# Performance work log

Hardware: AMD Instinct MI355X
Metric: run time of the kernel (lower is better)

The kernel has to match this reference:

```python
import jax, jax.numpy as jnp
import numpy as np
from functools import partial

WS, STRIDE, ALPHA, NHEADS = 8, 4, 0.3, 4


def _conv3x3(x, w, b):
    # x: [B,Cin,H,W], w: [Cout,Cin,3,3]
    y = jax.lax.conv_general_dilated(x, w, (1, 1), 'SAME',
                                     dimension_numbers=('NCHW', 'OIHW', 'NCHW'))
    return y + b[None, :, None, None]


def _conv1x1(x, w, b):
    y = jax.lax.conv_general_dilated(x, w, (1, 1), 'SAME',
                                     dimension_numbers=('NCHW', 'OIHW', 'NCHW'))
    return y + b[None, :, None, None]


def _mha(x, wqkv, bqkv, wo, bo):
    # x: [N, L, E] self-attention, torch nn.MultiheadAttention semantics
    N, L, E = x.shape
    hd = E // NHEADS
    qkv = x @ wqkv.T + bqkv                      # [N, L, 3E]
    q, k, v = jnp.split(qkv, 3, axis=-1)
    def heads(t):
        return t.reshape(N, L, NHEADS, hd).transpose(0, 2, 1, 3)  # [N,h,L,hd]
    q, k, v = heads(q) * (hd ** -0.5), heads(k), heads(v)
    attn = jax.nn.softmax(jnp.einsum('nhld,nhmd->nhlm', q, k), axis=-1)
    o = jnp.einsum('nhlm,nhmd->nhld', attn, v).transpose(0, 2, 1, 3).reshape(N, L, E)
    return o @ wo.T + bo


def _forward(vector_field, mw1, mb1, mw2, mb2, aw1, ab1, aw2, ab2,
             in_proj_w, in_proj_b, out_proj_w, out_proj_b, fc_w, fc_b):
    B, C_total, H, W = vector_field.shape
    C = C_total // 2
    E = 2 * C
    magnitudes = vector_field[:, :C]
    angles = vector_field[:, C:]

    mag_p = _conv3x3(jax.nn.relu(_conv3x3(magnitudes, mw1, mb1)), mw2, mb2)
    ang_p = _conv3x3(jax.nn.relu(_conv3x3(angles, aw1, ab1)), aw2, ab2)

    combined0 = jnp.concatenate([mag_p, ang_p], axis=1)      # [B, E, H, W]

    # ---- batched windowed cross-attention (windows read the ORIGINAL processed field) ----
    hs = np.arange(0, H - WS + 1, STRIDE)
    ws_ = np.arange(0, W - WS + 1, STRIDE)
    Nh, Nw = len(hs), len(ws_)
    rows = hs[:, None] + np.arange(WS)                        # [Nh, WS]
    cols = ws_[:, None] + np.arange(WS)                       # [Nw, WS]
    win = combined0[:, :, rows][:, :, :, :, cols]             # [B,E,Nh,WS,Nw,WS]
    tokens = win.transpose(2, 4, 0, 3, 5, 1).reshape(Nh * Nw * B, WS * WS, E)
    att = _mha(tokens, in_proj_w, in_proj_b, out_proj_w, out_proj_b)
    att = att.reshape(Nh * Nw, B, WS, WS, E).transpose(0, 1, 4, 2, 3)  # [NhNw,B,E,WS,WS]

    # ---- sequential read-modify-write blend (h outer, w inner loop order) ----
    h_idx = jnp.asarray(np.repeat(hs, Nw), dtype=jnp.int32)
    w_idx = jnp.asarray(np.tile(ws_, Nh), dtype=jnp.int32)

    def step(carry, inp):
        a, h0, w0 = inp
        cur = jax.lax.dynamic_slice(carry, (0, 0, h0, w0), (B, E, WS, WS))
        new = cur * (1.0 - ALPHA) + a * ALPHA
        return jax.lax.dynamic_update_slice(carry, new, (0, 0, h0, w0)), None

    enhanced, _ = jax.lax.scan(step, combined0, (att, h_idx, w_idx))

    enhanced_mag = enhanced[:, :C]
    enhanced_ang = enhanced[:, C:]

    flow_weights = jax.nn.sigmoid(_conv1x1(enhanced, fc_w, fc_b))  # [B,C,H,W]
    out = jnp.concatenate([enhanced_mag * flow_weights,
                           enhanced_ang * flow_weights], axis=1)
    return out + vector_field


def setup_inputs() -> dict:
    key = jax.random.key(0)
    ks = jax.random.split(key, 16)
    B, C, H, W = 4, 64, 128, 128
    E = 2 * C
    s = 0.05
    def n(k, shape):
        return jax.random.normal(k, shape, dtype=jnp.float32) * s
    return {
        'vector_field': jax.random.normal(ks[0], (B, 2 * C, H, W), dtype=jnp.float32),
        'mw1': n(ks[1], (C // 2, C, 3, 3)), 'mb1': n(ks[2], (C // 2,)),
        'mw2': n(ks[3], (C, C // 2, 3, 3)), 'mb2': n(ks[4], (C,)),
        'aw1': n(ks[5], (C // 2, C, 3, 3)), 'ab1': n(ks[6], (C // 2,)),
        'aw2': n(ks[7], (C, C // 2, 3, 3)), 'ab2': n(ks[8], (C,)),
        'in_proj_w': n(ks[9], (3 * E, E)), 'in_proj_b': n(ks[10], (3 * E,)),
        'out_proj_w': n(ks[11], (E, E)), 'out_proj_b': n(ks[12], (E,)),
        'fc_w': n(ks[13], (C, E, 1, 1)), 'fc_b': n(ks[14], (C,)),
    }


def reference(vector_field, mw1, mb1, mw2, mb2, aw1, ab1, aw2, ab2,
              in_proj_w, in_proj_b, out_proj_w, out_proj_b, fc_w, fc_b):
    return _forward(vector_field, mw1, mb1, mw2, mb2, aw1, ab1, aw2, ab2,
                    in_proj_w, in_proj_b, out_proj_w, out_proj_b, fc_w, fc_b)
```

## Files before the change

### kernel.cpp

```cpp
#include <hip/hip_runtime.h>
#include <hip/hip_bf16.h>


#define HW 16384
#define NSEQ 3844

#define WF_IPW 0
#define WF_IPB 49152
#define WF_OPW 49536
#define WF_OPB 65920
#define WF_FCW 66048
#define WF_FCB 74240
#define WF_MW1 74304
#define WF_MB1 92736
#define WF_AW1 92768
#define WF_AB1 111200
#define WF_MW2 111232
#define WF_MB2 129664
#define WF_AW2 129728
#define WF_AB2 148160
#define WF_TOTAL 148224
#define WF_W2BF 24576

typedef __bf16 bf16x8 __attribute__((ext_vector_type(8)));
typedef float f32x4 __attribute__((ext_vector_type(4)));
typedef unsigned int uint2v __attribute__((ext_vector_type(2)));
typedef unsigned int uint4v __attribute__((ext_vector_type(4)));

#define MFMA16(a, b, c) __builtin_amdgcn_mfma_f32_16x16x32_bf16((a), (b), (c), 0, 0, 0)

__device__ __forceinline__ float bfu(unsigned short u) {
    union { unsigned int i; float f; } v; v.i = ((unsigned int)u) << 16; return v.f;
}
__device__ __forceinline__ unsigned short fbf(float f) {
    union { float f; unsigned int i; } v; v.f = f;
    unsigned int x = v.i;
    return (unsigned short)((x + 0x7fffu + ((x >> 16) & 1u)) >> 16);
}
__device__ __forceinline__ unsigned int cvt_pk_bf16(float a, float b) {
    unsigned int r;
    asm("v_cvt_pk_bf16_f32 %0, %1, %2" : "=v"(r) : "v"(a), "v"(b));
    return r;
}
__device__ __forceinline__ unsigned short fbf_hw(float f) {
    return (unsigned short)cvt_pk_bf16(f, f);
}
__device__ __forceinline__ float ldin(const void* p, long long i, bool f32) {
    return f32 ? ((const float*)p)[i] : bfu(((const unsigned short*)p)[i]);
}
__device__ __forceinline__ bf16x8 frag_ld(const unsigned short* p) {
    union { uint4v u; bf16x8 b; } v;
    v.u = *(const uint4v*)p;
    return v.b;
}
__device__ __forceinline__ uint2v pack4(float a, float b, float c, float d) {
    uint2v r;
    r.x = cvt_pk_bf16(a, b);
    r.y = cvt_pk_bf16(c, d);
    return r;
}
__device__ __forceinline__ void unp8(uint4v u, float* x) {
    union { unsigned int i; float f; } a;
    a.i = u.x << 16;         x[0] = a.f;
    a.i = u.x & 0xffff0000u; x[1] = a.f;
    a.i = u.y << 16;         x[2] = a.f;
    a.i = u.y & 0xffff0000u; x[3] = a.f;
    a.i = u.z << 16;         x[4] = a.f;
    a.i = u.z & 0xffff0000u; x[5] = a.f;
    a.i = u.w << 16;         x[6] = a.f;
    a.i = u.w & 0xffff0000u; x[7] = a.f;
}

__global__ __launch_bounds__(256) void detect_kernel(const unsigned short* __restrict__ vfu,
                                                     int* __restrict__ flag)
{
    __shared__ int cnt;
    if (threadIdx.x == 0) cnt = 0;
    __syncthreads();
    int bad = 0;
    for (int i = threadIdx.x; i < 8192; i += 256) {
        int e = (vfu[i] >> 7) & 0xff;
        if (e < 0x60 || e > 0xA0) ++bad;
    }
    atomicAdd(&cnt, bad);
    __syncthreads();
    if (threadIdx.x == 0) *flag = (cnt > 400) ? 1 : 0;
}

__global__ __launch_bounds__(256) void cvtw_kernel(
    const void* ipw, const void* ipb,
    const void* opw, const void* opb,
    const void* fcw, const void* fcb,
    const void* mw1, const void* mb1,
    const void* aw1, const void* ab1,
    const void* mw2, const void* mb2,
    const void* aw2, const void* ab2,
    const int* __restrict__ flag, float* __restrict__ wf)
{
    int i = blockIdx.x * 256 + threadIdx.x;
    if (i >= WF_TOTAL) return;
    const bool f32 = (*flag != 0);
    const void* src; int off;
    if      (i < WF_IPB) { src = ipw; off = WF_IPW; }
    else if (i < WF_OPW) { src = ipb; off = WF_IPB; }
    else if (i < WF_OPB) { src = opw; off = WF_OPW; }
    else if (i < WF_FCW) { src = opb; off = WF_OPB; }
    else if (i < WF_FCB) { src = fcw; off = WF_FCW; }
    else if (i < WF_MW1) { src = fcb; off = WF_FCB; }
    else if (i < WF_MB1) { src = mw1; off = WF_MW1; }
    else if (i < WF_AW1) { src = mb1; off = WF_MB1; }
    else if (i < WF_AB1) { src = aw1; off = WF_AW1; }
    else if (i < WF_MB2) { src = (i < WF_MW2) ? ab1 : mw2; off = (i < WF_MW2) ? WF_AB1 : WF_MW2; }
    else if (i < WF_AW2) { src = mb2; off = WF_MB2; }
    else if (i < WF_AB2) { src = aw2; off = WF_AW2; }
    else                 { src = ab2; off = WF_AB2; }
    float v = ldin(src, i - off, f32);
    if (i < WF_IPB) {
        ((unsigned short*)(wf + WF_IPW))[i] = fbf(v);
    } else if (i >= WF_OPW && i < WF_OPB) {
        ((unsigned short*)(wf + WF_OPW))[i - WF_OPW] = fbf(v);
    } else {
        wf[i] = v;
    }
    if (i >= WF_MW2 && i < WF_MB2) {
        int rel = i - WF_MW2;
        int oc = rel / 288, rem = rel - oc * 288;
        int ic = rem / 9, tap = rem - ic * 9;
        ((unsigned short*)(wf + WF_W2BF))[oc * 288 + tap * 32 + ic] = fbf(v);
    } else if (i >= WF_AW2 && i < WF_AB2) {
        int rel = i - WF_AW2;
        int oc = rel / 288, rem = rel - oc * 288;
        int ic = rem / 9, tap = rem - ic * 9;
        ((unsigned short*)(wf + WF_W2BF))[18432 + oc * 288 + tap * 32 + ic] = fbf(v);
    }
}

template<int IC, bool RELU>
__device__ void conv3x3_body(const void* __restrict__ in, long long in_off, bool f32,
                             const float* __restrict__ w,
                             const float* __restrict__ bias,
                             unsigned short* __restrict__ out)
{
    __shared__ float xs[32][6][37];
    const int t = threadIdx.x;
    const int tx0 = blockIdx.x * 32, ty0 = blockIdx.y * 4;
    const int wv = __builtin_amdgcn_readfirstlane(t >> 6);
    const int lane = t & 63;
    const int pr = lane >> 4, pc2 = lane & 15;

    float acc[8][2];
#pragma unroll
    for (int oo = 0; oo < 8; ++oo)
#pragma unroll
        for (int p = 0; p < 2; ++p) acc[oo][p] = 0.f;

    for (int cc = 0; cc < IC; cc += 32) {
        if (cc) __syncthreads();
        for (int i = t; i < 32 * 108; i += 256) {
            int c = i / 108, rem = i - c * 108;
            int rr = rem / 18, s = rem - rr * 18;
            int gy = ty0 + rr - 1;
            const bool gyok = (gy >= 0 && gy < 128);
            long long rowoff = in_off + (long long)(cc + c) * HW + gy * 128;
            if (s >= 1 && s <= 16) {
                int cx = 2 * s - 1;
                int gx = tx0 + cx - 1;
                float v0 = 0.f, v1 = 0.f;
                if (gyok) {
                    if (f32) {
                        float2 u = *(const float2*)((const float*)in + rowoff + gx);
                        v0 = u.x; v1 = u.y;
                    } else {
                        unsigned int u = *(const unsigned int*)
                            ((const unsigned short*)in + rowoff + gx);
                        v0 = bfu((unsigned short)(u & 0xffffu));
                        v1 = bfu((unsigned short)(u >> 16));
                    }
                }
                xs[c][rr][cx] = v0;
                xs[c][rr][cx + 1] = v1;
            } else {
                int cx = (s == 0) ? 0 : 33;
                int gx = tx0 + cx - 1;
                float v = 0.f;
                if (gyok && gx >= 0 && gx < 128)
                    v = ldin(in, rowoff + gx, f32);
                xs[c][rr][cx] = v;
            }
        }
        __syncthreads();
        for (int c = 0; c < 32; ++c) {
            float xv[3][4];
#pragma unroll
            for (int dy = 0; dy < 3; ++dy)
#pragma unroll
                for (int dx = 0; dx < 4; ++dx)
                    xv[dy][dx] = xs[c][pr + dy][pc2 * 2 + dx];
            const float* wr0 = w + (wv * 8 * IC + (cc + c)) * 9;
#pragma unroll
            for (int oo = 0; oo < 8; ++oo) {
                const float* wr = wr0 + oo * IC * 9;
#pragma unroll
                for (int dy = 0; dy < 3; ++dy)
#pragma unroll
                    for (int dx = 0; dx < 3; ++dx) {
                        float wvv = wr[dy * 3 + dx];
#pragma unroll
                        for (int p = 0; p < 2; ++p)
                            acc[oo][p] = fmaf(wvv, xv[dy][p + dx], acc[oo][p]);
                    }
            }
        }
    }
    const int px = tx0 + pc2 * 2, py = ty0 + pr;
#pragma unroll
    for (int p = 0; p < 2; ++p) {
        union { unsigned int u32[4]; uint4v v; } pk;
#pragma unroll
        for (int j = 0; j < 4; ++j) {
            float v0 = acc[2 * j][p] + bias[wv * 8 + 2 * j];
            float v1 = acc[2 * j + 1][p] + bias[wv * 8 + 2 * j + 1];
            if (RELU) { v0 = fmaxf(v0, 0.f); v1 = fmaxf(v1, 0.f); }
            pk.u32[j] = cvt_pk_bf16(v0, v1);
        }
        *(uint4v*)(out + (size_t)(py * 128 + px + p) * 32 + wv * 8) = pk.v;
    }
}

__global__ __launch_bounds__(256) void conv1_kernel(const void* __restrict__ vf,
                                                    const float* __restrict__ wf,
                                                    const int* __restrict__ flag,
                                                    unsigned short* __restrict__ hidden)
{
    int z = blockIdx.z, b = z >> 1, br = z & 1;
    const bool f32 = (*flag != 0);
    conv3x3_body<64, true>(vf, (long long)(b * 128 + br * 64) * HW, f32,
                           wf + (br ? WF_AW1 : WF_MW1), wf + (br ? WF_AB1 : WF_MB1),
                           hidden + (size_t)z * 16384 * 32);
}

__global__ __launch_bounds__(256) void conv2_kernel(const unsigned short* __restrict__ hidden,
                                                    const float* __restrict__ wf,
                                                    unsigned short* __restrict__ comb)
{
    __shared__ unsigned short xs[8160];
    const int t = threadIdx.x;
    const int tx0 = blockIdx.x * 32, ty0 = blockIdx.y * 4;
    const int z = blockIdx.z, b = z >> 1, br = z & 1;
    const size_t ibase = (size_t)z * 16384;

    for (int i = t; i < 816; i += 256) {
        const int rec = i >> 2, part = i & 3;
        const int rr = rec / 34, cx = rec - rr * 34;
        const int gy = ty0 + rr - 1, gx = tx0 + cx - 1;
        uint4v v = {0u, 0u, 0u, 0u};
        if (gy >= 0 && gy < 128 && gx >= 0 && gx < 128)
            v = *(const uint4v*)(hidden + (ibase + gy * 128 + gx) * 32 + part * 8);
        *(uint4v*)&xs[rec * 40 + part * 8] = v;
    }
    __syncthreads();

    const int lane = t & 63, quad = lane >> 4, l16 = lane & 15;
    const int wv = __builtin_amdgcn_readfirstlane(t >> 6);
    const unsigned short* w2 = (const unsigned short*)(wf + WF_W2BF) + br * 18432;
    const float* bias = wf + (br ? WF_AB2 : WF_MB2);

    f32x4 acc[4][2];
#pragma unroll
    for (int oct = 0; oct < 4; ++oct) {
        f32x4 b4;
#pragma unroll
        for (int r = 0; r < 4; ++r) b4[r] = bias[oct * 16 + quad * 4 + r];
        acc[oct][0] = b4;
        acc[oct][1] = b4;
    }

    __builtin_amdgcn_s_setprio(1);
#pragma unroll
    for (int tap = 0; tap < 9; ++tap) {
        const int dy = tap / 3, dx = tap - dy * 3;
        bf16x8 bxf[2];
#pragma unroll
        for (int pt2 = 0; pt2 < 2; ++pt2)
            bxf[pt2] = frag_ld(&xs[((wv + dy) * 34 + (pt2 * 16 + l16 + dx)) * 40 + quad * 8]);
#pragma unroll
        for (int oct = 0; oct < 4; ++oct) {
            bf16x8 af = frag_ld(&w2[(oct * 16 + l16) * 288 + tap * 32 + quad * 8]);
            acc[oct][0] = MFMA16(af, bxf[0], acc[oct][0]);
            acc[oct][1] = MFMA16(af, bxf[1], acc[oct][1]);
        }
    }
    __builtin_amdgcn_s_setprio(0);

#pragma unroll
    for (int pt2 = 0; pt2 < 2; ++pt2) {
        const int px_ = tx0 + pt2 * 16 + l16;
        unsigned short* op = comb + ((size_t)b * 16384 + (ty0 + wv) * 128 + px_) * 128
                           + br * 64 + quad * 4;
#pragma unroll
        for (int oct = 0; oct < 4; ++oct)
            *(uint2v*)(op + oct * 16) =
                pack4(acc[oct][pt2][0], acc[oct][pt2][1],
                      acc[oct][pt2][2], acc[oct][pt2][3]);
    }
}

__global__ __launch_bounds__(256) void mha_kernel(
    const unsigned short* __restrict__ comb,
    const float* __restrict__ wf,
    unsigned short* __restrict__ att)
{
    __shared__ unsigned short lds[25088];

    const unsigned short* wqkv = (const unsigned short*)(wf + WF_IPW);
    const unsigned short* wo   = (const unsigned short*)(wf + WF_OPW);

    const int bid = blockIdx.x;
    const int xcd = bid & 7, idx = bid >> 3;
    const int start = (xcd < 4) ? xcd * 481 : 1924 + (xcd - 4) * 480;
    const int nl = start + idx;
    const int bb = nl / 961;
    const int ihw = nl - bb * 961;
    const int ih = ihw / 31, iw = ihw - ih * 31;
    const int n = ihw * 4 + bb;

    const int t = threadIdx.x;
    const int lane = t & 63, quad = lane >> 4, l16 = lane & 15;
    const int hh = __builtin_amdgcn_readfirstlane(t >> 6);
    const int hb = hh * 32;
    const int QOFF = 8704 + hh * 4096;
    const int KOFF = QOFF + 2048;
    const int VOFF = hh * 2048;

#pragma unroll
    for (int rh = 0; rh < 2; ++rh) {
        const int r = hh * 2 + rh;
        const unsigned short* rp = comb +
            (size_t)(bb * 16384 + (ih * 4 + r) * 128 + iw * 4) * 128;
#pragma unroll
        for (int hv = 0; hv < 2; ++hv) {
            uint4v v = *(const uint4v*)(rp + hv * 512 + lane * 8);
            const int tok = r * 8 + hv * 4 + (lane >> 4);
            *(uint4v*)&lds[tok * 136 + (lane & 15) * 8] = v;
        }
    }
    __syncthreads();

    {
        f32x4 acc[4][4];
#pragma unroll
        for (int nt = 0; nt < 4; ++nt) {
            const int rb = (nt < 2) ? (hb + nt * 16) : (128 + hb + (nt - 2) * 16);
            f32x4 b4;
            b4[0] = wf[WF_IPB + rb + quad * 4 + 0];
            b4[1] = wf[WF_IPB + rb + quad * 4 + 1];
            b4[2] = wf[WF_IPB + rb + quad * 4 + 2];
            b4[3] = wf[WF_IPB + rb + quad * 4 + 3];
#pragma unroll
            for (int mt = 0; mt < 4; ++mt) acc[nt][mt] = b4;
        }
        __builtin_amdgcn_s_setprio(1);
#pragma unroll
        for (int kc = 0; kc < 4; ++kc) {
            bf16x8 bx[4];
#pragma unroll
            for (int mt = 0; mt < 4; ++mt)
                bx[mt] = frag_ld(&lds[(mt * 16 + l16) * 136 + kc * 32 + quad * 8]);
#pragma unroll
            for (int nt = 0; nt < 4; ++nt) {
                const int rb = (nt < 2) ? (hb + nt * 16) : (128 + hb + (nt - 2) * 16);
                bf16x8 aw = frag_ld(&wqkv[(rb + l16) * 128 + kc * 32 + quad * 8]);
#pragma unroll
                for (int mt = 0; mt < 4; ++mt)
                    acc[nt][mt] = MFMA16(aw, bx[mt], acc[nt][mt]);
            }
        }
        __builtin_amdgcn_s_setprio(0);
#pragma unroll
        for (int nt = 0; nt < 2; ++nt)
#pragma unroll
            for (int mt = 0; mt < 4; ++mt) {
                const int tok = mt * 16 + l16;
                const int aoff = tok * 32 + (((nt * 2 + (quad >> 1)) ^ (tok & 3)) << 3)
                               + (quad & 1) * 4;
                *(uint2v*)&lds[QOFF + aoff] =
                    pack4(acc[nt][mt][0], acc[nt][mt][1], acc[nt][mt][2], acc[nt][mt][3]);
                *(uint2v*)&lds[KOFF + aoff] =
                    pack4(acc[nt + 2][mt][0], acc[nt + 2][mt][1],
                          acc[nt + 2][mt][2], acc[nt + 2][mt][3]);
            }
    }

    f32x4 accv[2][4];
#pragma unroll
    for (int nv = 0; nv < 2; ++nv) {
        const int rb = 256 + hb + nv * 16;
        f32x4 b4;
        b4[0] = wf[WF_IPB + rb + quad * 4 + 0];
        b4[1] = wf[WF_IPB + rb + quad * 4 + 1];
        b4[2] = wf[WF_IPB + rb + quad * 4 + 2];
        b4[3] = wf[WF_IPB + rb + quad * 4 + 3];
#pragma unroll
        for (int mt = 0; mt < 4; ++mt) accv[nv][mt] = b4;
    }
    __builtin_amdgcn_s_setprio(1);
#pragma unroll
    for (int kc = 0; kc < 4; ++kc) {
        bf16x8 bx[4];
#pragma unroll
        for (int mt = 0; mt < 4; ++mt)
            bx[mt] = frag_ld(&lds[(mt * 16 + l16) * 136 + kc * 32 + quad * 8]);
#pragma unroll
        for (int nv = 0; nv < 2; ++nv) {
            const int rb = 256 + hb + nv * 16;
            bf16x8 aw = frag_ld(&wqkv[(rb + l16) * 128 + kc * 32 + quad * 8]);
#pragma unroll
            for (int mt = 0; mt < 4; ++mt)
                accv[nv][mt] = MFMA16(aw, bx[mt], accv[nv][mt]);
        }
    }
    __builtin_amdgcn_s_setprio(0);
    __syncthreads();

#pragma unroll
    for (int nv = 0; nv < 2; ++nv)
#pragma unroll
        for (int mt = 0; mt < 4; ++mt)
#pragma unroll
            for (int r = 0; r < 4; ++r) {
                const int d = nv * 16 + quad * 4 + r;
                const int tok = mt * 16 + l16;
                lds[VOFF + d * 64 + (((tok >> 3) ^ (d & 7)) << 3) + (tok & 7)] =
                    fbf_hw(accv[nv][mt][r]);
            }

    bf16x8 ak[4], bq[4];
#pragma unroll
    for (int mtk = 0; mtk < 4; ++mtk) {
        const int tok = mtk * 16 + l16;
        ak[mtk] = frag_ld(&lds[KOFF + tok * 32 + ((quad ^ (tok & 3)) << 3)]);
    }
#pragma unroll
    for (int ntq = 0; ntq < 4; ++ntq) {
        const int tok = ntq * 16 + l16;
        bq[ntq] = frag_ld(&lds[QOFF + tok * 32 + ((quad ^ (tok & 3)) << 3)]);
    }
    f32x4 sc[4][4];
    {
        f32x4 zz = {0.f, 0.f, 0.f, 0.f};
        __builtin_amdgcn_s_setprio(1);
#pragma unroll
        for (int mtk = 0; mtk < 4; ++mtk)
#pragma unroll
            for (int ntq = 0; ntq < 4; ++ntq)
                sc[mtk][ntq] = MFMA16(ak[mtk], bq[ntq], zz);
        __builtin_amdgcn_s_setprio(0);
    }

    const float scale = 0.17677669529663687f;
#pragma unroll
    for (int ntq = 0; ntq < 4; ++ntq) {
        float m0 = -1e30f;
#pragma unroll
        for (int mtk = 0; mtk < 4; ++mtk)
#pragma unroll
            for (int r = 0; r < 4; ++r) {
                sc[mtk][ntq][r] *= scale;
                m0 = fmaxf(m0, sc[mtk][ntq][r]);
            }
        m0 = fmaxf(m0, __shfl_xor(m0, 16));
        m0 = fmaxf(m0, __shfl_xor(m0, 32));
        float s0 = 0.f;
#pragma unroll
        for (int mtk = 0; mtk < 4; ++mtk)
#pragma unroll
            for (int r = 0; r < 4; ++r) {
                float p = __expf(sc[mtk][ntq][r] - m0);
                sc[mtk][ntq][r] = p;
                s0 += p;
            }
        s0 += __shfl_xor(s0, 16);
        s0 += __shfl_xor(s0, 32);
        float inv = 1.f / s0;
        const int tokq = ntq * 16 + l16;
#pragma unroll
        for (int mtk = 0; mtk < 4; ++mtk)
            *(uint2v*)&lds[QOFF + tokq * 64 +
                           (((mtk * 2 + (quad >> 1)) ^ (tokq & 7)) << 3) + (quad & 1) * 4] =
                pack4(sc[mtk][ntq][0] * inv, sc[mtk][ntq][1] * inv,
                      sc[mtk][ntq][2] * inv, sc[mtk][ntq][3] * inv);
    }
    __asm__ volatile("s_waitcnt lgkmcnt(0)" ::: "memory");

    f32x4 ov[4][2];
#pragma unroll
    for (int mt = 0; mt < 4; ++mt)
#pragma unroll
        for (int nv = 0; nv < 2; ++nv) { f32x4 zz = {0.f, 0.f, 0.f, 0.f}; ov[mt][nv] = zz; }
    __builtin_amdgcn_s_setprio(1);
#pragma unroll
    for (int ks = 0; ks < 2; ++ks) {
        bf16x8 ap[4];
#pragma unroll
        for (int mt = 0; mt < 4; ++mt) {
            const int tokq = mt * 16 + l16;
            ap[mt] = frag_ld(&lds[QOFF + tokq * 64 + (((ks * 4 + quad) ^ (tokq & 7)) << 3)]);
        }
#pragma unroll
        for (int nv = 0; nv < 2; ++nv) {
            const int d = nv * 16 + l16;
            bf16x8 bv = frag_ld(&lds[VOFF + d * 64 + (((ks * 4 + quad) ^ (d & 7)) << 3)]);
#pragma unroll
            for (int mt = 0; mt < 4; ++mt)
                ov[mt][nv] = MFMA16(ap[mt], bv, ov[mt][nv]);
        }
    }
    __builtin_amdgcn_s_setprio(0);
    __syncthreads();

#pragma unroll
    for (int mt = 0; mt < 4; ++mt)
#pragma unroll
        for (int nv = 0; nv < 2; ++nv)
#pragma unroll
            for (int r = 0; r < 4; ++r)
                lds[(mt * 16 + quad * 4 + r) * 136 + hb + nv * 16 + l16] =
                    fbf_hw(ov[mt][nv][r]);
    __syncthreads();

    f32x4 dp[4][2];
#pragma unroll
    for (int mt = 0; mt < 4; ++mt)
#pragma unroll
        for (int nl = 0; nl < 2; ++nl) { f32x4 zz = {0.f, 0.f, 0.f, 0.f}; dp[mt][nl] = zz; }
    __builtin_amdgcn_s_setprio(1);
#pragma unroll
    for (int ks = 0; ks < 4; ++ks) {
        bf16x8 af[4];
#pragma unroll
        for (int mt = 0; mt < 4; ++mt)
            af[mt] = frag_ld(&lds[(mt * 16 + l16) * 136 + ks * 32 + quad * 8]);
#pragma unroll
        for (int nl = 0; nl < 2; ++nl) {
            const int erow = hb + nl * 16 + l16;
            bf16x8 bw = frag_ld(&wo[erow * 128 + ks * 32 + quad * 8]);
#pragma unroll
            for (int mt = 0; mt < 4; ++mt)
                dp[mt][nl] = MFMA16(af[mt], bw, dp[mt][nl]);
        }
    }
    __builtin_amdgcn_s_setprio(0);
    __syncthreads();

#pragma unroll
    for (int mt = 0; mt < 4; ++mt)
#pragma unroll
        for (int nl = 0; nl < 2; ++nl)
#pragma unroll
            for (int r = 0; r < 4; ++r)
                lds[(mt * 16 + quad * 4 + r) * 136 + hb + nl * 16 + l16] =
                    fbf_hw(dp[mt][nl][r]);
    __syncthreads();

    {
        const int tok2 = t >> 2, eo = (t & 3) * 32;
        unsigned short* op = att + (size_t)n * 8192 + tok2 * 128 + eo;
        const unsigned short* lp = lds + tok2 * 136 + eo;
#pragma unroll
        for (int k4 = 0; k4 < 4; ++k4)
            *(uint4v*)(op + k4 * 8) = *(const uint4v*)(lp + k4 * 8);
    }
}

__global__ __launch_bounds__(256) void fuse_kernel(
    const unsigned short* __restrict__ comb,
    const unsigned short* __restrict__ att,
    const void* __restrict__ vf,
    const float* __restrict__ wf,
    const int* __restrict__ flag,
    void* __restrict__ outp)
{
    __shared__ float enhs[128][65];
    __shared__ float fws[64][65];
    const float* fcw = wf + WF_FCW;
    const float* fcb = wf + WF_FCB;
    const bool f32 = (*flag != 0);
    const int t = threadIdx.x;
    const int wl = t & 63;
    const int eg = __builtin_amdgcn_readfirstlane(t >> 6);
    const int h = blockIdx.y, b = blockIdx.z;
    const int w = blockIdx.x * 64 + wl;

    const int mh = h >> 2, mw = w >> 2;
    const bool vh0 = (mh >= 1), vh1 = (mh <= 30);
    const bool vw0 = (mw >= 1), vw1 = (mw <= 30);
    const int k = ((int)vh0 + (int)vh1) * ((int)vw0 + (int)vw1);
    const float base7 = (k == 1) ? 0.7f : (k == 2) ? 0.49f : 0.2401f;
    const float bias_c = 1.f - base7;

    float cw[4]; int coff[4];
    {
        const bool vs[4] = { vh0 && vw0, vh0 && vw1, vh1 && vw0, vh1 && vw1 };
        const int ihc[4] = { mh - 1, mh - 1, mh, mh };
        const int iwc[4] = { mw - 1, mw, mw - 1, mw };
        int j = 0;
#pragma unroll
        for (int s = 0; s < 4; ++s) {
            if (vs[s]) {
                ++j;
                int e2 = k - j;
                float pw = (e2 == 0) ? 1.f : (e2 == 1) ? 0.7f : (e2 == 2) ? 0.49f : 0.343f;
                cw[s] = 0.3f * pw;
                int nn = (ihc[s] * 31 + iwc[s]) * 4 + b;
                int ll = (h - 4 * ihc[s]) * 8 + (w - 4 * iwc[s]);
                coff[s] = nn * 8192 + ll * 128;
            } else { cw[s] = 0.f; coff[s] = 0; }
        }
    }

    const int cbase = (b * 128) * HW + h * 128 + w;
    const size_t cpix = (size_t)(b * 16384 + h * 128 + w) * 128;
    const int e0 = eg * 32;
#pragma unroll
    for (int i8 = 0; i8 < 4; ++i8) {
        float av[8];
#pragma unroll
        for (int j = 0; j < 8; ++j)
            av[j] = bias_c * wf[WF_OPB + e0 + i8 * 8 + j];
#pragma unroll
        for (int s = 0; s < 4; ++s) {
            uint4v u = *(const uint4v*)(att + coff[s] + e0 + i8 * 8);
            float x[8];
            unp8(u, x);
#pragma unroll
            for (int j = 0; j < 8; ++j)
                av[j] = fmaf(cw[s], x[j], av[j]);
        }
        uint4v cu = *(const uint4v*)(comb + cpix + e0 + i8 * 8);
        float cx[8];
        unp8(cu, cx);
#pragma unroll
        for (int j = 0; j < 8; ++j)
            enhs[e0 + i8 * 8 + j][wl] = fmaf(base7, cx[j], av[j]);
    }
    __syncthreads();

    float a2[16];
    const int co0 = eg * 16;
#pragma unroll
    for (int i = 0; i < 16; ++i) a2[i] = fcb[co0 + i];
    const float4* fcw4 = (const float4*)fcw;
    for (int eb = 0; eb < 32; ++eb) {
        float x0 = enhs[eb * 4 + 0][wl];
        float x1 = enhs[eb * 4 + 1][wl];
        float x2 = enhs[eb * 4 + 2][wl];
        float x3 = enhs[eb * 4 + 3][wl];
#pragma unroll
        for (int i = 0; i < 16; ++i) {
            float4 wv4 = fcw4[(co0 + i) * 32 + eb];
            float a = a2[i];
            a = fmaf(x0, wv4.x, a);
            a = fmaf(x1, wv4.y, a);
            a = fmaf(x2, wv4.z, a);
            a = fmaf(x3, wv4.w, a);
            a2[i] = a;
        }
    }
#pragma unroll
    for (int i = 0; i < 16; ++i)
        fws[co0 + i][wl] = 1.f / (1.f + __expf(-a2[i]));
    __syncthreads();

#pragma unroll
    for (int i = 0; i < 32; ++i) {
        const int e = eg * 32 + i;
        const int idx = cbase + e * HW;
        float val = enhs[e][wl] * fws[e & 63][wl] + ldin(vf, idx, f32);
        if (f32) ((float*)outp)[idx] = val;
        else     ((unsigned short*)outp)[idx] = fbf_hw(val);
    }
}

extern "C" void kernel_launch(void* const* d_in, const int* in_sizes, int n_in,
                              void* d_out, int out_size, void* d_ws, size_t ws_size,
                              hipStream_t stream)
{
    const void* vf  = d_in[0];
    const void* mw1 = d_in[1];
    const void* mb1 = d_in[2];
    const void* mw2 = d_in[3];
    const void* mb2 = d_in[4];
    const void* aw1 = d_in[5];
    const void* ab1 = d_in[6];
    const void* aw2 = d_in[7];
    const void* ab2 = d_in[8];
    const void* ipw = d_in[9];
    const void* ipb = d_in[10];
    const void* opw = d_in[11];
    const void* opb = d_in[12];
    const void* fcw = d_in[13];
    const void* fcb = d_in[14];

    int* flag = (int*)d_ws;
    float* wf = (float*)((char*)d_ws + 1024);
    unsigned short* comb = (unsigned short*)((char*)d_ws + 593920);
    unsigned short* hidden = (unsigned short*)((char*)d_ws + 17371136);
    unsigned short* att = (unsigned short*)((char*)d_ws + 17371136);

    detect_kernel<<<1, 256, 0, stream>>>((const unsigned short*)vf, flag);
    cvtw_kernel<<<(WF_TOTAL + 255) / 256, 256, 0, stream>>>(
        ipw, ipb, opw, opb, fcw, fcb, mw1, mb1, aw1, ab1, mw2, mb2, aw2, ab2, flag, wf);
    conv1_kernel<<<dim3(4, 32, 8), 256, 0, stream>>>(vf, wf, flag, hidden);
    conv2_kernel<<<dim3(4, 32, 8), 256, 0, stream>>>(hidden, wf, comb);
    mha_kernel<<<NSEQ, 256, 0, stream>>>(comb, wf, att);
    fuse_kernel<<<dim3(2, 128, 4), 256, 0, stream>>>(comb, att, vf, wf, flag, d_out);
}
```

Measured before the change: 344.5 us.

## Run first 3x3 conv on bf16 MFMA with a channel-last pre-transposed input

Adds a kernel that transposes the input field into a pixel-major, channel-last bf16 buffer, and reorders the conv1 weights into bf16 tap-major layout. conv1 is rewritten to use 16x16 MFMA instructions over 9 taps and two 32-channel chunks, replacing the scalar FP32 FMA loop. The intent is to move the first convolution from vector ALU onto the matrix cores. In exchange it adds an extra kernel launch, an intermediate buffer write and read, and bf16 rounding of the input.

```diff
diff --git a/kernel.cpp b/kernel.cpp
--- a/kernel.cpp
+++ b/kernel.cpp
@@ -119,6 +119,16 @@
         ((unsigned short*)(wf + WF_IPW))[i] = fbf(v);
     } else if (i >= WF_OPW && i < WF_OPB) {
         ((unsigned short*)(wf + WF_OPW))[i - WF_OPW] = fbf(v);
+    } else if (i >= WF_MW1 && i < WF_MB1) {
+        int rel = i - WF_MW1;
+        int oc = rel / 576, rem = rel - oc * 576;
+        int ic = rem / 9, tap = rem - ic * 9;
+        ((unsigned short*)(wf + WF_MW1))[oc * 576 + tap * 64 + ic] = fbf(v);
+    } else if (i >= WF_AW1 && i < WF_AB1) {
+        int rel = i - WF_AW1;
+        int oc = rel / 576, rem = rel - oc * 576;
+        int ic = rem / 9, tap = rem - ic * 9;
+        ((unsigned short*)(wf + WF_AW1))[oc * 576 + tap * 64 + ic] = fbf(v);
     } else {
         wf[i] = v;
     }
@@ -135,108 +145,105 @@
     }
 }
 
-template<int IC, bool RELU>
-__device__ void conv3x3_body(const void* __restrict__ in, long long in_off, bool f32,
-                             const float* __restrict__ w,
-                             const float* __restrict__ bias,
-                             unsigned short* __restrict__ out)
+__global__ __launch_bounds__(256) void vf2p_kernel(const void* __restrict__ vf,
+                                                   const int* __restrict__ flag,
+                                                   unsigned short* __restrict__ vfp)
 {
-    __shared__ float xs[32][6][37];
+    __shared__ unsigned short ts[64 * 72];
+    const int t = threadIdx.x;
+    const int z = blockIdx.y;
+    const int px0 = blockIdx.x * 64;
+    const bool f32 = (*flag != 0);
+    const long long in_off = (long long)((z >> 1) * 128 + (z & 1) * 64) * HW;
+
+    for (int i = t; i < 2048; i += 256) {
+        const int c = i >> 5, jp = i & 31;
+        const long long a = in_off + (long long)c * HW + px0 + 2 * jp;
+        if (f32) {
+            float2 u = *(const float2*)((const float*)vf + a);
+            ts[(2 * jp) * 72 + c] = fbf_hw(u.x);
+            ts[(2 * jp + 1) * 72 + c] = fbf_hw(u.y);
+        } else {
+            unsigned int u = *(const unsigned int*)((const unsigned short*)vf + a);
+            ts[(2 * jp) * 72 + c] = (unsigned short)(u & 0xffffu);
+            ts[(2 * jp + 1) * 72 + c] = (unsigned short)(u >> 16);
+        }
+    }
+    __syncthreads();
+    for (int i = t; i < 512; i += 256) {
+        const int px = i >> 3, part = i & 7;
+        *(uint4v*)(vfp + ((size_t)z * 16384 + px0 + px) * 64 + part * 8) =
+            *(const uint4v*)&ts[px * 72 + part * 8];
+    }
+}
+
+__global__ __launch_bounds__(256) void conv1_kernel(const unsigned short* __restrict__ vfp,
+                                                    const float* __restrict__ wf,
+                                                    unsigned short* __restrict__ hidden)
+{
+    __shared__ unsigned short xs[8160];
     const int t = threadIdx.x;
     const int tx0 = blockIdx.x * 32, ty0 = blockIdx.y * 4;
+    const int z = blockIdx.z, br = z & 1;
+    const size_t ibase = (size_t)z * 16384;
+
+    const int lane = t & 63, quad = lane >> 4, l16 = lane & 15;
     const int wv = __builtin_amdgcn_readfirstlane(t >> 6);
-    const int lane = t & 63;
-    const int pr = lane >> 4, pc2 = lane & 15;
-
-    float acc[8][2];
-#pragma unroll
-    for (int oo = 0; oo < 8; ++oo)
-#pragma unroll
-        for (int p = 0; p < 2; ++p) acc[oo][p] = 0.f;
-
-    for (int cc = 0; cc < IC; cc += 32) {
-        if (cc) __syncthreads();
-        for (int i = t; i < 32 * 108; i += 256) {
-            int c = i / 108, rem = i - c * 108;
-            int rr = rem / 18, s = rem - rr * 18;
-            int gy = ty0 + rr - 1;
-            const bool gyok = (gy >= 0 && gy < 128);
-            long long rowoff = in_off + (long long)(cc + c) * HW + gy * 128;
-            if (s >= 1 && s <= 16) {
-                int cx = 2 * s - 1;
-                int gx = tx0 + cx - 1;
-                float v0 = 0.f, v1 = 0.f;
-                if (gyok) {
-                    if (f32) {
-                        float2 u = *(const float2*)((const float*)in + rowoff + gx);
-                        v0 = u.x; v1 = u.y;
-                    } else {
-                        unsigned int u = *(const unsigned int*)
-                            ((const unsigned short*)in + rowoff + gx);
-                        v0 = bfu((unsigned short)(u & 0xffffu));
-                        v1 = bfu((unsigned short)(u >> 16));
-                    }
-                }
-                xs[c][rr][cx] = v0;
-                xs[c][rr][cx + 1] = v1;
-            } else {
-                int cx = (s == 0) ? 0 : 33;
-                int gx = tx0 + cx - 1;
-                float v = 0.f;
-                if (gyok && gx >= 0 && gx < 128)
-                    v = ldin(in, rowoff + gx, f32);
-                xs[c][rr][cx] = v;
+    const unsigned short* w1 = (const unsigned short*)(wf + (br ? WF_AW1 : WF_MW1));
+    const float* bias = wf + (br ? WF_AB1 : WF_MB1);
+
+    f32x4 acc[2][2];
+#pragma unroll
+    for (int oct = 0; oct < 2; ++oct) {
+        f32x4 b4;
+#pragma unroll
+        for (int r = 0; r < 4; ++r) b4[r] = bias[oct * 16 + quad * 4 + r];
+        acc[oct][0] = b4;
+        acc[oct][1] = b4;
+    }
+
+    for (int ck = 0; ck < 2; ++ck) {
+        if (ck) __syncthreads();
+        for (int i = t; i < 816; i += 256) {
+            const int rec = i >> 2, part = i & 3;
+            const int rr = rec / 34, cx = rec - rr * 34;
+            const int gy = ty0 + rr - 1, gx = tx0 + cx - 1;
+            uint4v v = {0u, 0u, 0u, 0u};
+            if (gy >= 0 && gy < 128 && gx >= 0 && gx < 128)
+                v = *(const uint4v*)(vfp + (ibase + gy * 128 + gx) * 64 + ck * 32 + part * 8);
+            *(uint4v*)&xs[rec * 40 + part * 8] = v;
+        }
+        __syncthreads();
+        __builtin_amdgcn_s_setprio(1);
+#pragma unroll
+        for (int tap = 0; tap < 9; ++tap) {
+            const int dy = tap / 3, dx = tap - dy * 3;
+            bf16x8 bxf[2];
+#pragma unroll
+            for (int pt2 = 0; pt2 < 2; ++pt2)
+                bxf[pt2] = frag_ld(&xs[((wv + dy) * 34 + (pt2 * 16 + l16 + dx)) * 40 + quad * 8]);
+#pragma unroll
+            for (int oct = 0; oct < 2; ++oct) {
+                bf16x8 af = frag_ld(&w1[(oct * 16 + l16) * 576 + tap * 64 + ck * 32 + quad * 8]);
+                acc[oct][0] = MFMA16(af, bxf[0], acc[oct][0]);
+                acc[oct][1] = MFMA16(af, bxf[1], acc[oct][1]);
             }
         }
-        __syncthreads();
-        for (int c = 0; c < 32; ++c) {
-            float xv[3][4];
-#pragma unroll
-            for (int dy = 0; dy < 3; ++dy)
-#pragma unroll
-                for (int dx = 0; dx < 4; ++dx)
-                    xv[dy][dx] = xs[c][pr + dy][pc2 * 2 + dx];
-            const float* wr0 = w + (wv * 8 * IC + (cc + c)) * 9;
-#pragma unroll
-            for (int oo = 0; oo < 8; ++oo) {
-                const float* wr = wr0 + oo * IC * 9;
-#pragma unroll
-                for (int dy = 0; dy < 3; ++dy)
-#pragma unroll
-                    for (int dx = 0; dx < 3; ++dx) {
-                        float wvv = wr[dy * 3 + dx];
-#pragma unroll
-                        for (int p = 0; p < 2; ++p)
-                            acc[oo][p] = fmaf(wvv, xv[dy][p + dx], acc[oo][p]);
-                    }
-            }
-        }
-    }
-    const int px = tx0 + pc2 * 2, py = ty0 + pr;
-#pragma unroll
-    for (int p = 0; p < 2; ++p) {
-        union { unsigned int u32[4]; uint4v v; } pk;
-#pragma unroll
-        for (int j = 0; j < 4; ++j) {
-            float v0 = acc[2 * j][p] + bias[wv * 8 + 2 * j];
-            float v1 = acc[2 * j + 1][p] + bias[wv * 8 + 2 * j + 1];
-            if (RELU) { v0 = fmaxf(v0, 0.f); v1 = fmaxf(v1, 0.f); }
-            pk.u32[j] = cvt_pk_bf16(v0, v1);
-        }
-        *(uint4v*)(out + (size_t)(py * 128 + px + p) * 32 + wv * 8) = pk.v;
-    }
-}
-
-__global__ __launch_bounds__(256) void conv1_kernel(const void* __restrict__ vf,
-                                                    const float* __restrict__ wf,
-                                                    const int* __restrict__ flag,
-                                                    unsigned short* __restrict__ hidden)
-{
-    int z = blockIdx.z, b = z >> 1, br = z & 1;
-    const bool f32 = (*flag != 0);
-    conv3x3_body<64, true>(vf, (long long)(b * 128 + br * 64) * HW, f32,
-                           wf + (br ? WF_AW1 : WF_MW1), wf + (br ? WF_AB1 : WF_MB1),
-                           hidden + (size_t)z * 16384 * 32);
+        __builtin_amdgcn_s_setprio(0);
+    }
+
+#pragma unroll
+    for (int pt2 = 0; pt2 < 2; ++pt2) {
+        const int px_ = tx0 + pt2 * 16 + l16;
+        unsigned short* op = hidden + (ibase + (ty0 + wv) * 128 + px_) * 32 + quad * 4;
+#pragma unroll
+        for (int oct = 0; oct < 2; ++oct) {
+            f32x4 a = acc[oct][pt2];
+            *(uint2v*)(op + oct * 16) =
+                pack4(fmaxf(a[0], 0.f), fmaxf(a[1], 0.f),
+                      fmaxf(a[2], 0.f), fmaxf(a[3], 0.f));
+        }
+    }
 }
 
 __global__ __launch_bounds__(256) void conv2_kernel(const unsigned short* __restrict__ hidden,
@@ -704,13 +711,15 @@
     int* flag = (int*)d_ws;
     float* wf = (float*)((char*)d_ws + 1024);
     unsigned short* comb = (unsigned short*)((char*)d_ws + 593920);
-    unsigned short* hidden = (unsigned short*)((char*)d_ws + 17371136);
+    unsigned short* vfp = (unsigned short*)((char*)d_ws + 17371136);
+    unsigned short* hidden = (unsigned short*)((char*)d_ws + 34148352);
     unsigned short* att = (unsigned short*)((char*)d_ws + 17371136);
 
     detect_kernel<<<1, 256, 0, stream>>>((const unsigned short*)vf, flag);
     cvtw_kernel<<<(WF_TOTAL + 255) / 256, 256, 0, stream>>>(
         ipw, ipb, opw, opb, fcw, fcb, mw1, mb1, aw1, ab1, mw2, mb2, aw2, ab2, flag, wf);
-    conv1_kernel<<<dim3(4, 32, 8), 256, 0, stream>>>(vf, wf, flag, hidden);
+    vf2p_kernel<<<dim3(256, 8), 256, 0, stream>>>(vf, flag, vfp);
+    conv1_kernel<<<dim3(4, 32, 8), 256, 0, stream>>>(vfp, wf, hidden);
     conv2_kernel<<<dim3(4, 32, 8), 256, 0, stream>>>(hidden, wf, comb);
     mha_kernel<<<NSEQ, 256, 0, stream>>>(comb, wf, att);
     fuse_kernel<<<dim3(2, 128, 4), 256, 0, stream>>>(comb, att, vf, wf, flag, d_out);
```

Result: faster. 303.7 us (-11.8%).
